# Performance work log

Hardware: AMD Instinct MI355X
Metric: run time of the kernel (lower is better)

## Reference

```python
import jax, jax.numpy as jnp
import numpy as np

NU, NM, D, E = 100000, 20000, 128, 1000000


def _seg_mean(feats, idx, n):
    # scatter-mean: zero for nodes with no incoming edges (PyG semantics)
    s = jax.ops.segment_sum(feats, idx, num_segments=n)
    c = jax.ops.segment_sum(jnp.ones((idx.shape[0], 1), feats.dtype), idx, num_segments=n)
    return s / jnp.maximum(c, 1.0)


def _hetero_sage(xu, xm, e_src, e_dst, Wl_um, Wr_um, b_um, Wl_mu, Wr_mu, b_mu):
    # ('user','rates','movie'): aggregate user features at movies
    agg_m = _seg_mean(xu[e_src], e_dst, xm.shape[0])          # [Nm, D]
    out_m = agg_m @ Wl_um + b_um + xm @ Wr_um                  # [Nm, H]
    # ('movie','rev_rates','user'): aggregate movie features at users
    agg_u = _seg_mean(xm[e_dst], e_src, xu.shape[0])          # [Nu, D]
    out_u = agg_u @ Wl_mu + b_mu + xu @ Wr_mu                  # [Nu, H]
    return out_u, out_m


def setup_inputs() -> dict:
    key = jax.random.key(0)
    ks = jax.random.split(key, 20)
    glorot = lambda k: (jax.random.normal(k, (D, D), jnp.float32) / np.sqrt(D)).astype(jnp.float32)
    inp = {
        "x_user": jax.random.normal(ks[0], (NU, D), jnp.float32),
        "x_movie": jax.random.normal(ks[1], (NM, D), jnp.float32),
        "edge_src": jax.random.randint(ks[2], (E,), 0, NU),
        "edge_dst": jax.random.randint(ks[3], (E,), 0, NM),
    }
    names = ["Wl1_um", "Wr1_um", "Wl1_mu", "Wr1_mu", "Wl2_um", "Wr2_um", "Wl2_mu", "Wr2_mu"]
    for i, n in enumerate(names):
        inp[n] = glorot(ks[4 + i])
    inp["b1_um"] = jnp.zeros((D,), jnp.float32)
    inp["b1_mu"] = jnp.zeros((D,), jnp.float32)
    inp["b2_um"] = jnp.zeros((D,), jnp.float32)
    inp["b2_mu"] = jnp.zeros((D,), jnp.float32)
    return inp


def reference(x_user, x_movie, Wl1_um, Wr1_um, Wl1_mu, Wr1_mu, Wl2_um, Wr2_um, Wl2_mu, Wr2_mu, b1_um, b1_mu, b2_um, b2_mu, edge_src, edge_dst):
    # layer 1 + relu (dropout = identity in eval) + residual
    h1_u, h1_m = _hetero_sage(x_user, x_movie, edge_src, edge_dst,
                              Wl1_um, Wr1_um, b1_um, Wl1_mu, Wr1_mu, b1_mu)
    r_u = x_user + jax.nn.relu(h1_u)
    r_m = x_movie + jax.nn.relu(h1_m)
    # layer 2 (dropout = identity in eval)
    out_u, out_m = _hetero_sage(r_u, r_m, edge_src, edge_dst,
                                Wl2_um, Wr2_um, b2_um, Wl2_mu, Wr2_mu, b2_mu)
    return out_u, out_m
```

## Files before the change

kernel.cpp:

```cpp
#include <hip/hip_runtime.h>
#include <stdint.h>

typedef unsigned short u16;
typedef unsigned int u32;
typedef __attribute__((ext_vector_type(8))) short short8;
typedef __attribute__((ext_vector_type(4))) float f32x4;

__device__ __forceinline__ u16 f2bf(float f) {
    u32 x = __float_as_uint(f);
    u32 r = x + 0x7FFFu + ((x >> 16) & 1u);
    return (u16)(r >> 16);
}
__device__ __forceinline__ u32 pack2bf(float a, float b) {
    return (u32)f2bf(a) | ((u32)f2bf(b) << 16);
}
__device__ __forceinline__ float bflo(u32 w) { return __uint_as_float(w << 16); }
__device__ __forceinline__ float bfhi(u32 w) { return __uint_as_float(w & 0xFFFF0000u); }

__global__ __launch_bounds__(256)
void hist_rank(const int* __restrict__ src, const int* __restrict__ dst,
               int* __restrict__ cnt, int* __restrict__ ranku,
               int* __restrict__ rankm, int E, int nu, int nm) {
    int e = blockIdx.x * 256 + threadIdx.x;
    if (e >= E) return;
    int s = src[e], d = dst[e];
    if ((unsigned)s < (unsigned)nu && (unsigned)d < (unsigned)nm) {
        ranku[e] = atomicAdd(&cnt[s], 1);
        rankm[e] = atomicAdd(&cnt[nu + d], 1);
    } else {
        ranku[e] = -1;
    }
}

__global__ __launch_bounds__(256)
void scan_partial(const int* __restrict__ cnt, int* __restrict__ bsum, int n) {
    __shared__ int s[256];
    const int tid = threadIdx.x;
    int base = blockIdx.x * 4096 + tid * 16;
    int sum = 0;
#pragma unroll
    for (int k = 0; k < 16; ++k) {
        int i = base + k;
        if (i < n) sum += cnt[i];
    }
    s[tid] = sum;
    __syncthreads();
    for (int d = 128; d > 0; d >>= 1) {
        if (tid < d) s[tid] += s[tid + d];
        __syncthreads();
    }
    if (tid == 0) bsum[blockIdx.x] = s[0];
}

__global__ __launch_bounds__(64)
void scan_top(int* __restrict__ bsum, int nb, int* __restrict__ off, int n) {
    if (threadIdx.x == 0) {
        int run = 0;
        for (int b = 0; b < nb; ++b) { int v = bsum[b]; bsum[b] = run; run += v; }
        off[n] = run;
    }
}

__global__ __launch_bounds__(256)
void scan_apply(const int* __restrict__ cnt, const int* __restrict__ bsum,
                int* __restrict__ off, int n) {
    __shared__ int s[256];
    const int tid = threadIdx.x;
    int base = blockIdx.x * 4096 + tid * 16;
    int v[16];
    int sum = 0;
#pragma unroll
    for (int k = 0; k < 16; ++k) {
        int i = base + k;
        v[k] = (i < n) ? cnt[i] : 0;
        sum += v[k];
    }
    s[tid] = sum;
    __syncthreads();
    for (int d = 1; d < 256; d <<= 1) {
        int t = (tid >= d) ? s[tid - d] : 0;
        __syncthreads();
        s[tid] += t;
        __syncthreads();
    }
    int run = bsum[blockIdx.x] + s[tid] - sum;
#pragma unroll
    for (int k = 0; k < 16; ++k) {
        int i = base + k;
        if (i < n) off[i] = run;
        run += v[k];
    }
}

__global__ __launch_bounds__(256)
void fill_pos(const int* __restrict__ src, const int* __restrict__ dst,
              const int* __restrict__ ranku, const int* __restrict__ rankm,
              const int* __restrict__ off, int* __restrict__ nbr,
              int E, int nu) {
    int e = blockIdx.x * 256 + threadIdx.x;
    if (e >= E) return;
    int ru = ranku[e];
    if (ru < 0) return;
    int s = src[e], d = dst[e];
    nbr[off[s] + ru] = d;
    nbr[off[nu + d] + rankm[e]] = s;
}

__global__ __launch_bounds__(256)
void to_bf16(const float* __restrict__ in, u32* __restrict__ out, int n64) {
    int i = blockIdx.x * 256 + threadIdx.x;
    if (i < n64) {
        float2 v = ((const float2*)in)[i];
        out[i] = pack2bf(v.x, v.y);
    }
}

__global__ __launch_bounds__(64)
void wprep(const float* __restrict__ Wl, const float* __restrict__ Wr,
           u16* __restrict__ out) {
    const int bid = blockIdx.x;
    const int t = bid >> 3, s = bid & 7;
    const int lane = threadIdx.x;
    const int n = t * 16 + (lane & 15);
    const int k0 = s * 32 + (lane >> 4) * 8;
    u16 v[8];
#pragma unroll
    for (int j = 0; j < 8; ++j) {
        int k = k0 + j;
        float f = (k < 128) ? Wl[k * 128 + n] : Wr[(k - 128) * 128 + n];
        v[j] = f2bf(f);
    }
    *(short8*)(out + ((size_t)(t * 8 + s) * 64 + lane) * 8) = *(short8*)v;
}

template <int L1>
__global__ __launch_bounds__(256)
void fused_update(const u32* __restrict__ featb, const float* __restrict__ xf,
                  const u32* __restrict__ xb,
                  const int* __restrict__ off, const int* __restrict__ nbr,
                  const u16* __restrict__ wt, const float* __restrict__ bias,
                  void* __restrict__ outp, int N) {
    __shared__ u32 sVb[16][132];
    __shared__ float sX[16][130];
    const int tid = threadIdx.x;
    const int lane = tid & 63;
    const int wave = tid >> 6;
    const int base = blockIdx.x * 16;

    for (int c = 0; c < 4; ++c) {
        const int i = wave * 4 + c;
        const int n = base + i;
        if (n < N) {
            const int b = off[n], e = off[n + 1];
            float a0x = 0.f, a0y = 0.f, a1x = 0.f, a1y = 0.f;
            float a2x = 0.f, a2y = 0.f, a3x = 0.f, a3y = 0.f;
            int t = b;
            for (; t + 3 < e; t += 4) {
                int g0 = nbr[t], g1 = nbr[t + 1], g2 = nbr[t + 2], g3 = nbr[t + 3];
                u32 w0 = featb[(size_t)g0 * 64 + lane];
                u32 w1 = featb[(size_t)g1 * 64 + lane];
                u32 w2 = featb[(size_t)g2 * 64 + lane];
                u32 w3 = featb[(size_t)g3 * 64 + lane];
                a0x += bflo(w0); a0y += bfhi(w0);
                a1x += bflo(w1); a1y += bfhi(w1);
                a2x += bflo(w2); a2y += bfhi(w2);
                a3x += bflo(w3); a3y += bfhi(w3);
            }
            for (; t < e; ++t) {
                u32 w = featb[(size_t)nbr[t] * 64 + lane];
                a0x += bflo(w); a0y += bfhi(w);
            }
            const int dg = e - b;
            const float inv = 1.0f / (float)(dg > 1 ? dg : 1);
            const float mx = (a0x + a1x + a2x + a3x) * inv;
            const float my = (a0y + a1y + a2y + a3y) * inv;
            sVb[i][lane] = pack2bf(mx, my);
            if (L1) {
                const float2 xv = ((const float2*)xf)[(size_t)n * 64 + lane];
                sVb[i][64 + lane] = pack2bf(xv.x, xv.y);
                sX[i][2 * lane] = xv.x;
                sX[i][2 * lane + 1] = xv.y;
            } else {
                sVb[i][64 + lane] = xb[(size_t)n * 64 + lane];
            }
        } else {
            sVb[i][lane] = 0u;
            sVb[i][64 + lane] = 0u;
            if (L1) { sX[i][2 * lane] = 0.f; sX[i][2 * lane + 1] = 0.f; }
        }
    }
    __syncthreads();

    const int ml = lane & 15;
    const int quad = lane >> 4;
    const int t0 = wave * 2, t1 = wave * 2 + 1;
    const u16* sVbu = (const u16*)sVb;
    const short8* wtp = (const short8*)wt;

    f32x4 acc0 = {0.f, 0.f, 0.f, 0.f};
    f32x4 acc1 = {0.f, 0.f, 0.f, 0.f};
#pragma unroll
    for (int s = 0; s < 8; ++s) {
        short8 a = *(const short8*)(sVbu + (size_t)ml * 264 + s * 32 + quad * 8);
        short8 b0 = wtp[(size_t)(t0 * 8 + s) * 64 + lane];
        short8 b1 = wtp[(size_t)(t1 * 8 + s) * 64 + lane];
        acc0 = __builtin_amdgcn_mfma_f32_16x16x32_bf16(a, b0, acc0, 0, 0, 0);
        acc1 = __builtin_amdgcn_mfma_f32_16x16x32_bf16(a, b1, acc1, 0, 0, 0);
    }

    const int n0 = t0 * 16 + ml, n1 = t1 * 16 + ml;
    const float bj0 = bias[n0], bj1 = bias[n1];
#pragma unroll
    for (int r = 0; r < 4; ++r) {
        const int m = quad * 4 + r;
        const int node = base + m;
        if (node < N) {
            float h0 = acc0[r] + bj0;
            float h1 = acc1[r] + bj1;
            if (L1) {
                u16* ob = (u16*)outp;
                ob[(size_t)node * 128 + n0] = f2bf(sX[m][n0] + fmaxf(h0, 0.f));
                ob[(size_t)node * 128 + n1] = f2bf(sX[m][n1] + fmaxf(h1, 0.f));
            } else {
                float* o = (float*)outp;
                o[(size_t)node * 128 + n0] = h0;
                o[(size_t)node * 128 + n1] = h1;
            }
        }
    }
}

extern "C" void kernel_launch(void* const* d_in, const int* in_sizes, int n_in,
                              void* d_out, int out_size, void* d_ws, size_t ws_size,
                              hipStream_t stream) {
    const int nu = in_sizes[0] / 128;
    const int nm = in_sizes[1] / 128;
    const int E = in_sizes[2];

    const float* xu = (const float*)d_in[0];
    const float* xm = (const float*)d_in[1];
    const int* esrc = (const int*)d_in[2];
    const int* edst = (const int*)d_in[3];
    const float* Wl1_um = (const float*)d_in[4];
    const float* Wr1_um = (const float*)d_in[5];
    const float* Wl1_mu = (const float*)d_in[6];
    const float* Wr1_mu = (const float*)d_in[7];
    const float* Wl2_um = (const float*)d_in[8];
    const float* Wr2_um = (const float*)d_in[9];
    const float* Wl2_mu = (const float*)d_in[10];
    const float* Wr2_mu = (const float*)d_in[11];
    const float* b1_um = (const float*)d_in[12];
    const float* b1_mu = (const float*)d_in[13];
    const float* b2_um = (const float*)d_in[14];
    const float* b2_mu = (const float*)d_in[15];

    float* out_u = (float*)d_out;
    float* out_m = out_u + (size_t)nu * 128;

    const int ntot = nu + nm;
    const int NB = (ntot + 4095) / 4096;
    int* cnt = (int*)d_ws;
    int* off = cnt + ntot;
    int* bsum = off + ntot + 1;
    int* ranku = bsum + ((NB + 15) & ~15);
    int* rankm = ranku + E;
    int* nbr = rankm + E;
    size_t int_bytes = (size_t)((nbr + 2 * (size_t)E) - (int*)d_ws) * 4;
    size_t wt_off = (int_bytes + 63) & ~(size_t)63;
    u16* wt1_um = (u16*)((char*)d_ws + wt_off);
    u16* wt1_mu = wt1_um + 32768;
    u16* wt2_um = wt1_mu + 32768;
    u16* wt2_mu = wt2_um + 32768;
    u32* Abf = (u32*)((char*)d_ws + wt_off + 4 * 65536);
    u32* xmb = Abf + (size_t)nu * 64;
    u32* rmb = xmb + (size_t)nm * 64;

    const int eg = (E + 255) / 256;

    wprep<<<64, 64, 0, stream>>>(Wl1_um, Wr1_um, wt1_um);
    wprep<<<64, 64, 0, stream>>>(Wl1_mu, Wr1_mu, wt1_mu);
    wprep<<<64, 64, 0, stream>>>(Wl2_um, Wr2_um, wt2_um);
    wprep<<<64, 64, 0, stream>>>(Wl2_mu, Wr2_mu, wt2_mu);
    to_bf16<<<(nu * 64 + 255) / 256, 256, 0, stream>>>(xu, Abf, nu * 64);
    to_bf16<<<(nm * 64 + 255) / 256, 256, 0, stream>>>(xm, xmb, nm * 64);

    hipMemsetAsync(cnt, 0, (size_t)ntot * 4, stream);
    hist_rank<<<eg, 256, 0, stream>>>(esrc, edst, cnt, ranku, rankm, E, nu, nm);
    scan_partial<<<NB, 256, 0, stream>>>(cnt, bsum, ntot);
    scan_top<<<1, 64, 0, stream>>>(bsum, NB, off, ntot);
    scan_apply<<<NB, 256, 0, stream>>>(cnt, bsum, off, ntot);
    fill_pos<<<eg, 256, 0, stream>>>(esrc, edst, ranku, rankm, off, nbr, E, nu);

    const int gm = (nm + 15) / 16;
    const int gu = (nu + 15) / 16;

    fused_update<1><<<gm, 256, 0, stream>>>(
        Abf, xm, nullptr, off + nu, nbr, wt1_um, b1_um, rmb, nm);
    fused_update<1><<<gu, 256, 0, stream>>>(
        xmb, xu, nullptr, off, nbr, wt1_mu, b1_mu, Abf, nu);

    fused_update<0><<<gm, 256, 0, stream>>>(
        Abf, nullptr, rmb, off + nu, nbr, wt2_um, b2_um, out_m, nm);
    fused_update<0><<<gu, 256, 0, stream>>>(
        rmb, nullptr, Abf, off, nbr, wt2_mu, b2_mu, out_u, nu);
}
```

Before: 570.7 us.

## Merge prep kernels, drop scan_top, vectorize gather, 32-node tiles, dual layer-2 launch

Folds histogram, bf16 conversion and weight packing into one prep launch. The scan's top level is now computed redundantly inside scan_apply, which assumes at most 64 partial blocks. The neighbor gather now uses 16-byte loads with four edges per wave in parallel plus a shuffle reduction, and each block handles 32 nodes with four MFMA accumulators. The two layer-2 updates share one launch. The main target is launch overhead and gather memory efficiency, at the cost of more registers and an fp32 re-read of x in the layer-1 epilogue.

```diff
diff --git a/kernel.cpp b/kernel.cpp
--- a/kernel.cpp
+++ b/kernel.cpp
@@ -5,6 +5,7 @@
 typedef unsigned int u32;
 typedef __attribute__((ext_vector_type(8))) short short8;
 typedef __attribute__((ext_vector_type(4))) float f32x4;
+typedef __attribute__((ext_vector_type(4))) u32 u32x4;
 
 __device__ __forceinline__ u16 f2bf(float f) {
     u32 x = __float_as_uint(f);
@@ -17,18 +18,67 @@
 __device__ __forceinline__ float bflo(u32 w) { return __uint_as_float(w << 16); }
 __device__ __forceinline__ float bfhi(u32 w) { return __uint_as_float(w & 0xFFFF0000u); }
 
-__global__ __launch_bounds__(256)
-void hist_rank(const int* __restrict__ src, const int* __restrict__ dst,
-               int* __restrict__ cnt, int* __restrict__ ranku,
-               int* __restrict__ rankm, int E, int nu, int nm) {
-    int e = blockIdx.x * 256 + threadIdx.x;
-    if (e >= E) return;
-    int s = src[e], d = dst[e];
-    if ((unsigned)s < (unsigned)nu && (unsigned)d < (unsigned)nm) {
-        ranku[e] = atomicAdd(&cnt[s], 1);
-        rankm[e] = atomicAdd(&cnt[nu + d], 1);
+struct WPtrs {
+    const float* wl[4];
+    const float* wr[4];
+    u16* wout[4];
+};
+
+__global__ __launch_bounds__(256)
+void prep_kernel(const int* __restrict__ src, const int* __restrict__ dst,
+                 int* __restrict__ cnt, int* __restrict__ ranku,
+                 int* __restrict__ rankm, int E, int nu, int nm,
+                 const float* __restrict__ xu, const float* __restrict__ xm,
+                 u32* __restrict__ xub, u32* __restrict__ xmb,
+                 int eg, int cg, WPtrs wp) {
+    const int bid = blockIdx.x;
+    const int tid = threadIdx.x;
+    if (bid < eg) {
+        int e = bid * 256 + tid;
+        if (e < E) {
+            int s = src[e], d = dst[e];
+            if ((unsigned)s < (unsigned)nu && (unsigned)d < (unsigned)nm) {
+                ranku[e] = atomicAdd(&cnt[s], 1);
+                rankm[e] = atomicAdd(&cnt[nu + d], 1);
+            } else {
+                ranku[e] = -1;
+            }
+        }
+    } else if (bid < eg + cg) {
+        const int id = (bid - eg) * 1024 + tid * 4;
+        const int nuc = nu * 64;
+        const int tot = nuc + nm * 64;
+        if (id < tot) {
+            const float* fin;
+            u32* fout;
+            int rel;
+            if (id < nuc) { fin = xu; fout = xub; rel = id; }
+            else          { fin = xm; fout = xmb; rel = id - nuc; }
+            float4 p0 = ((const float4*)fin)[(rel >> 1)];
+            float4 p1 = ((const float4*)fin)[(rel >> 1) + 1];
+            u32x4 o = { pack2bf(p0.x, p0.y), pack2bf(p0.z, p0.w),
+                        pack2bf(p1.x, p1.y), pack2bf(p1.z, p1.w) };
+            *(u32x4*)(fout + rel) = o;
+        }
     } else {
-        ranku[e] = -1;
+        const int unit = (bid - eg - cg) * 4 + (tid >> 6);
+        if (unit < 256) {
+            const int stack = unit >> 6, r = unit & 63, t = r >> 3, s = r & 7;
+            const int lane = tid & 63;
+            const float* Wl = wp.wl[stack];
+            const float* Wr = wp.wr[stack];
+            u16* outw = wp.wout[stack];
+            const int n = t * 16 + (lane & 15);
+            const int k0 = s * 32 + (lane >> 4) * 8;
+            u16 v[8];
+#pragma unroll
+            for (int j = 0; j < 8; ++j) {
+                int k = k0 + j;
+                float f = (k < 128) ? Wl[k * 128 + n] : Wr[(k - 128) * 128 + n];
+                v[j] = f2bf(f);
+            }
+            *(short8*)(outw + ((size_t)(t * 8 + s) * 64 + lane) * 8) = *(short8*)v;
+        }
     }
 }
 
@@ -52,19 +102,12 @@
     if (tid == 0) bsum[blockIdx.x] = s[0];
 }
 
-__global__ __launch_bounds__(64)
-void scan_top(int* __restrict__ bsum, int nb, int* __restrict__ off, int n) {
-    if (threadIdx.x == 0) {
-        int run = 0;
-        for (int b = 0; b < nb; ++b) { int v = bsum[b]; bsum[b] = run; run += v; }
-        off[n] = run;
-    }
-}
-
 __global__ __launch_bounds__(256)
 void scan_apply(const int* __restrict__ cnt, const int* __restrict__ bsum,
-                int* __restrict__ off, int n) {
+                int* __restrict__ off, int n, int nb) {
     __shared__ int s[256];
+    __shared__ int sb[64];
+    __shared__ int pfx;
     const int tid = threadIdx.x;
     int base = blockIdx.x * 4096 + tid * 16;
     int v[16];
@@ -76,6 +119,7 @@
         sum += v[k];
     }
     s[tid] = sum;
+    if (tid < 64) sb[tid] = (tid < nb) ? bsum[tid] : 0;
     __syncthreads();
     for (int d = 1; d < 256; d <<= 1) {
         int t = (tid >= d) ? s[tid - d] : 0;
@@ -83,7 +127,14 @@
         s[tid] += t;
         __syncthreads();
     }
-    int run = bsum[blockIdx.x] + s[tid] - sum;
+    if (tid == 0) {
+        int p = 0;
+        for (int b2 = 0; b2 < (int)blockIdx.x; ++b2) p += sb[b2];
+        pfx = p;
+        if ((int)blockIdx.x == nb - 1) off[n] = p + s[255];
+    }
+    __syncthreads();
+    int run = pfx + s[tid] - sum;
 #pragma unroll
     for (int k = 0; k < 16; ++k) {
         int i = base + k;
@@ -106,128 +157,152 @@
     nbr[off[nu + d] + rankm[e]] = s;
 }
 
-__global__ __launch_bounds__(256)
-void to_bf16(const float* __restrict__ in, u32* __restrict__ out, int n64) {
-    int i = blockIdx.x * 256 + threadIdx.x;
-    if (i < n64) {
-        float2 v = ((const float2*)in)[i];
-        out[i] = pack2bf(v.x, v.y);
-    }
-}
-
-__global__ __launch_bounds__(64)
-void wprep(const float* __restrict__ Wl, const float* __restrict__ Wr,
-           u16* __restrict__ out) {
-    const int bid = blockIdx.x;
-    const int t = bid >> 3, s = bid & 7;
-    const int lane = threadIdx.x;
-    const int n = t * 16 + (lane & 15);
-    const int k0 = s * 32 + (lane >> 4) * 8;
-    u16 v[8];
-#pragma unroll
-    for (int j = 0; j < 8; ++j) {
-        int k = k0 + j;
-        float f = (k < 128) ? Wl[k * 128 + n] : Wr[(k - 128) * 128 + n];
-        v[j] = f2bf(f);
-    }
-    *(short8*)(out + ((size_t)(t * 8 + s) * 64 + lane) * 8) = *(short8*)v;
-}
-
 template <int L1>
-__global__ __launch_bounds__(256)
-void fused_update(const u32* __restrict__ featb, const float* __restrict__ xf,
-                  const u32* __restrict__ xb,
-                  const int* __restrict__ off, const int* __restrict__ nbr,
-                  const u16* __restrict__ wt, const float* __restrict__ bias,
-                  void* __restrict__ outp, int N) {
-    __shared__ u32 sVb[16][132];
-    __shared__ float sX[16][130];
+__device__ __forceinline__ void fused_body(
+    const u32* __restrict__ featb, const float* __restrict__ xf,
+    const u32* __restrict__ xb, const int* __restrict__ off,
+    const int* __restrict__ nbr, const u16* __restrict__ wt,
+    const float* __restrict__ bias, void* __restrict__ outp, int N, int blk) {
+    __shared__ u32 sVb[32][132];
     const int tid = threadIdx.x;
     const int lane = tid & 63;
     const int wave = tid >> 6;
-    const int base = blockIdx.x * 16;
-
-    for (int c = 0; c < 4; ++c) {
-        const int i = wave * 4 + c;
+    const int base = blk * 32;
+    const int q = lane >> 4;
+    const int cl = lane & 15;
+
+    for (int c = 0; c < 8; ++c) {
+        const int i = wave * 8 + c;
         const int n = base + i;
         if (n < N) {
             const int b = off[n], e = off[n + 1];
-            float a0x = 0.f, a0y = 0.f, a1x = 0.f, a1y = 0.f;
-            float a2x = 0.f, a2y = 0.f, a3x = 0.f, a3y = 0.f;
+            float a0 = 0.f, a1 = 0.f, a2 = 0.f, a3 = 0.f;
+            float a4 = 0.f, a5 = 0.f, a6 = 0.f, a7 = 0.f;
             int t = b;
-            for (; t + 3 < e; t += 4) {
-                int g0 = nbr[t], g1 = nbr[t + 1], g2 = nbr[t + 2], g3 = nbr[t + 3];
-                u32 w0 = featb[(size_t)g0 * 64 + lane];
-                u32 w1 = featb[(size_t)g1 * 64 + lane];
-                u32 w2 = featb[(size_t)g2 * 64 + lane];
-                u32 w3 = featb[(size_t)g3 * 64 + lane];
-                a0x += bflo(w0); a0y += bfhi(w0);
-                a1x += bflo(w1); a1y += bfhi(w1);
-                a2x += bflo(w2); a2y += bfhi(w2);
-                a3x += bflo(w3); a3y += bfhi(w3);
-            }
-            for (; t < e; ++t) {
-                u32 w = featb[(size_t)nbr[t] * 64 + lane];
-                a0x += bflo(w); a0y += bfhi(w);
-            }
+            for (; t + 15 < e; t += 16) {
+                int g0 = nbr[t + q];
+                int g1 = nbr[t + 4 + q];
+                int g2 = nbr[t + 8 + q];
+                int g3 = nbr[t + 12 + q];
+                u32x4 v0 = *(const u32x4*)(featb + (size_t)g0 * 64 + cl * 4);
+                u32x4 v1 = *(const u32x4*)(featb + (size_t)g1 * 64 + cl * 4);
+                u32x4 v2 = *(const u32x4*)(featb + (size_t)g2 * 64 + cl * 4);
+                u32x4 v3 = *(const u32x4*)(featb + (size_t)g3 * 64 + cl * 4);
+                a0 += bflo(v0.x); a1 += bfhi(v0.x); a2 += bflo(v0.y); a3 += bfhi(v0.y);
+                a4 += bflo(v0.z); a5 += bfhi(v0.z); a6 += bflo(v0.w); a7 += bfhi(v0.w);
+                a0 += bflo(v1.x); a1 += bfhi(v1.x); a2 += bflo(v1.y); a3 += bfhi(v1.y);
+                a4 += bflo(v1.z); a5 += bfhi(v1.z); a6 += bflo(v1.w); a7 += bfhi(v1.w);
+                a0 += bflo(v2.x); a1 += bfhi(v2.x); a2 += bflo(v2.y); a3 += bfhi(v2.y);
+                a4 += bflo(v2.z); a5 += bfhi(v2.z); a6 += bflo(v2.w); a7 += bfhi(v2.w);
+                a0 += bflo(v3.x); a1 += bfhi(v3.x); a2 += bflo(v3.y); a3 += bfhi(v3.y);
+                a4 += bflo(v3.z); a5 += bfhi(v3.z); a6 += bflo(v3.w); a7 += bfhi(v3.w);
+            }
+            for (; t < e; t += 4) {
+                int it = t + q;
+                if (it < e) {
+                    u32x4 v = *(const u32x4*)(featb + (size_t)nbr[it] * 64 + cl * 4);
+                    a0 += bflo(v.x); a1 += bfhi(v.x); a2 += bflo(v.y); a3 += bfhi(v.y);
+                    a4 += bflo(v.z); a5 += bfhi(v.z); a6 += bflo(v.w); a7 += bfhi(v.w);
+                }
+            }
+            a0 += __shfl_xor(a0, 16); a0 += __shfl_xor(a0, 32);
+            a1 += __shfl_xor(a1, 16); a1 += __shfl_xor(a1, 32);
+            a2 += __shfl_xor(a2, 16); a2 += __shfl_xor(a2, 32);
+            a3 += __shfl_xor(a3, 16); a3 += __shfl_xor(a3, 32);
+            a4 += __shfl_xor(a4, 16); a4 += __shfl_xor(a4, 32);
+            a5 += __shfl_xor(a5, 16); a5 += __shfl_xor(a5, 32);
+            a6 += __shfl_xor(a6, 16); a6 += __shfl_xor(a6, 32);
+            a7 += __shfl_xor(a7, 16); a7 += __shfl_xor(a7, 32);
             const int dg = e - b;
             const float inv = 1.0f / (float)(dg > 1 ? dg : 1);
-            const float mx = (a0x + a1x + a2x + a3x) * inv;
-            const float my = (a0y + a1y + a2y + a3y) * inv;
-            sVb[i][lane] = pack2bf(mx, my);
+            if (q == 0) {
+                u32x4 o = { pack2bf(a0 * inv, a1 * inv), pack2bf(a2 * inv, a3 * inv),
+                            pack2bf(a4 * inv, a5 * inv), pack2bf(a6 * inv, a7 * inv) };
+                *(u32x4*)&sVb[i][cl * 4] = o;
+            }
             if (L1) {
                 const float2 xv = ((const float2*)xf)[(size_t)n * 64 + lane];
                 sVb[i][64 + lane] = pack2bf(xv.x, xv.y);
-                sX[i][2 * lane] = xv.x;
-                sX[i][2 * lane + 1] = xv.y;
             } else {
                 sVb[i][64 + lane] = xb[(size_t)n * 64 + lane];
             }
         } else {
             sVb[i][lane] = 0u;
             sVb[i][64 + lane] = 0u;
-            if (L1) { sX[i][2 * lane] = 0.f; sX[i][2 * lane + 1] = 0.f; }
         }
     }
     __syncthreads();
 
-    const int ml = lane & 15;
-    const int quad = lane >> 4;
-    const int t0 = wave * 2, t1 = wave * 2 + 1;
+    const int t0 = wave * 2, t1 = t0 + 1;
     const u16* sVbu = (const u16*)sVb;
     const short8* wtp = (const short8*)wt;
 
-    f32x4 acc0 = {0.f, 0.f, 0.f, 0.f};
-    f32x4 acc1 = {0.f, 0.f, 0.f, 0.f};
+    f32x4 acc00 = {0.f, 0.f, 0.f, 0.f};
+    f32x4 acc01 = {0.f, 0.f, 0.f, 0.f};
+    f32x4 acc10 = {0.f, 0.f, 0.f, 0.f};
+    f32x4 acc11 = {0.f, 0.f, 0.f, 0.f};
 #pragma unroll
     for (int s = 0; s < 8; ++s) {
-        short8 a = *(const short8*)(sVbu + (size_t)ml * 264 + s * 32 + quad * 8);
+        short8 a0 = *(const short8*)(sVbu + (size_t)cl * 264 + s * 32 + q * 8);
+        short8 a1 = *(const short8*)(sVbu + (size_t)(16 + cl) * 264 + s * 32 + q * 8);
         short8 b0 = wtp[(size_t)(t0 * 8 + s) * 64 + lane];
         short8 b1 = wtp[(size_t)(t1 * 8 + s) * 64 + lane];
-        acc0 = __builtin_amdgcn_mfma_f32_16x16x32_bf16(a, b0, acc0, 0, 0, 0);
-        acc1 = __builtin_amdgcn_mfma_f32_16x16x32_bf16(a, b1, acc1, 0, 0, 0);
-    }
-
-    const int n0 = t0 * 16 + ml, n1 = t1 * 16 + ml;
+        acc00 = __builtin_amdgcn_mfma_f32_16x16x32_bf16(a0, b0, acc00, 0, 0, 0);
+        acc01 = __builtin_amdgcn_mfma_f32_16x16x32_bf16(a0, b1, acc01, 0, 0, 0);
+        acc10 = __builtin_amdgcn_mfma_f32_16x16x32_bf16(a1, b0, acc10, 0, 0, 0);
+        acc11 = __builtin_amdgcn_mfma_f32_16x16x32_bf16(a1, b1, acc11, 0, 0, 0);
+    }
+
+    const int n0 = t0 * 16 + cl, n1 = t1 * 16 + cl;
     const float bj0 = bias[n0], bj1 = bias[n1];
 #pragma unroll
-    for (int r = 0; r < 4; ++r) {
-        const int m = quad * 4 + r;
-        const int node = base + m;
-        if (node < N) {
-            float h0 = acc0[r] + bj0;
-            float h1 = acc1[r] + bj1;
-            if (L1) {
-                u16* ob = (u16*)outp;
-                ob[(size_t)node * 128 + n0] = f2bf(sX[m][n0] + fmaxf(h0, 0.f));
-                ob[(size_t)node * 128 + n1] = f2bf(sX[m][n1] + fmaxf(h1, 0.f));
-            } else {
-                float* o = (float*)outp;
-                o[(size_t)node * 128 + n0] = h0;
-                o[(size_t)node * 128 + n1] = h1;
-            }
-        }
-    }
+    for (int mt = 0; mt < 2; ++mt) {
+        const f32x4& c0 = mt ? acc10 : acc00;
+        const f32x4& c1 = mt ? acc11 : acc01;
+#pragma unroll
+        for (int r = 0; r < 4; ++r) {
+            const int m = mt * 16 + q * 4 + r;
+            const int node = base + m;
+            if (node < N) {
+                float h0 = c0[r] + bj0;
+                float h1 = c1[r] + bj1;
+                if (L1) {
+                    u16* ob = (u16*)outp;
+                    float x0 = xf[(size_t)node * 128 + n0];
+                    float x1 = xf[(size_t)node * 128 + n1];
+                    ob[(size_t)node * 128 + n0] = f2bf(x0 + fmaxf(h0, 0.f));
+                    ob[(size_t)node * 128 + n1] = f2bf(x1 + fmaxf(h1, 0.f));
+                } else {
+                    float* o = (float*)outp;
+                    o[(size_t)node * 128 + n0] = h0;
+                    o[(size_t)node * 128 + n1] = h1;
+                }
+            }
+        }
+    }
+}
+
+__global__ __launch_bounds__(256)
+void fused_l1(const u32* __restrict__ featb, const float* __restrict__ xf,
+              const int* __restrict__ off, const int* __restrict__ nbr,
+              const u16* __restrict__ wt, const float* __restrict__ bias,
+              void* __restrict__ outp, int N) {
+    fused_body<1>(featb, xf, nullptr, off, nbr, wt, bias, outp, N, blockIdx.x);
+}
+
+__global__ __launch_bounds__(256)
+void fused_l2_dual(const u32* __restrict__ Abf, const u32* __restrict__ rmb,
+                   const int* __restrict__ off, const int* __restrict__ nbr,
+                   const u16* __restrict__ wtm, const u16* __restrict__ wtu,
+                   const float* __restrict__ bm, const float* __restrict__ bu,
+                   float* __restrict__ outm, float* __restrict__ outu,
+                   int nm, int nu, int gm) {
+    if ((int)blockIdx.x < gm)
+        fused_body<0>(Abf, nullptr, rmb, off + nu, nbr, wtm, bm, outm, nm,
+                      blockIdx.x);
+    else
+        fused_body<0>(rmb, nullptr, Abf, off, nbr, wtu, bu, outu, nu,
+                      blockIdx.x - gm);
 }
 
 extern "C" void kernel_launch(void* const* d_in, const int* in_sizes, int n_in,
@@ -276,31 +351,30 @@
     u32* rmb = xmb + (size_t)nm * 64;
 
     const int eg = (E + 255) / 256;
-
-    wprep<<<64, 64, 0, stream>>>(Wl1_um, Wr1_um, wt1_um);
-    wprep<<<64, 64, 0, stream>>>(Wl1_mu, Wr1_mu, wt1_mu);
-    wprep<<<64, 64, 0, stream>>>(Wl2_um, Wr2_um, wt2_um);
-    wprep<<<64, 64, 0, stream>>>(Wl2_mu, Wr2_mu, wt2_mu);
-    to_bf16<<<(nu * 64 + 255) / 256, 256, 0, stream>>>(xu, Abf, nu * 64);
-    to_bf16<<<(nm * 64 + 255) / 256, 256, 0, stream>>>(xm, xmb, nm * 64);
+    const int cg = ((nu + nm) * 64 + 1023) / 1024;
+
+    WPtrs wp;
+    wp.wl[0] = Wl1_um; wp.wr[0] = Wr1_um; wp.wout[0] = wt1_um;
+    wp.wl[1] = Wl1_mu; wp.wr[1] = Wr1_mu; wp.wout[1] = wt1_mu;
+    wp.wl[2] = Wl2_um; wp.wr[2] = Wr2_um; wp.wout[2] = wt2_um;
+    wp.wl[3] = Wl2_mu; wp.wr[3] = Wr2_mu; wp.wout[3] = wt2_mu;
 
     hipMemsetAsync(cnt, 0, (size_t)ntot * 4, stream);
-    hist_rank<<<eg, 256, 0, stream>>>(esrc, edst, cnt, ranku, rankm, E, nu, nm);
+    prep_kernel<<<eg + cg + 64, 256, 0, stream>>>(
+        esrc, edst, cnt, ranku, rankm, E, nu, nm, xu, xm, Abf, xmb, eg, cg, wp);
     scan_partial<<<NB, 256, 0, stream>>>(cnt, bsum, ntot);
-    scan_top<<<1, 64, 0, stream>>>(bsum, NB, off, ntot);
-    scan_apply<<<NB, 256, 0, stream>>>(cnt, bsum, off, ntot);
+    scan_apply<<<NB, 256, 0, stream>>>(cnt, bsum, off, ntot, NB);
     fill_pos<<<eg, 256, 0, stream>>>(esrc, edst, ranku, rankm, off, nbr, E, nu);
 
-    const int gm = (nm + 15) / 16;
-    const int gu = (nu + 15) / 16;
-
-    fused_update<1><<<gm, 256, 0, stream>>>(
-        Abf, xm, nullptr, off + nu, nbr, wt1_um, b1_um, rmb, nm);
-    fused_update<1><<<gu, 256, 0, stream>>>(
-        xmb, xu, nullptr, off, nbr, wt1_mu, b1_mu, Abf, nu);
-
-    fused_update<0><<<gm, 256, 0, stream>>>(
-        Abf, nullptr, rmb, off + nu, nbr, wt2_um, b2_um, out_m, nm);
-    fused_update<0><<<gu, 256, 0, stream>>>(
-        rmb, nullptr, Abf, off, nbr, wt2_mu, b2_mu, out_u, nu);
-}
+    const int gm = (nm + 31) / 32;
+    const int gu = (nu + 31) / 32;
+
+    fused_l1<<<gm, 256, 0, stream>>>(Abf, xm, off + nu, nbr, wt1_um, b1_um,
+                                     rmb, nm);
+    fused_l1<<<gu, 256, 0, stream>>>(xmb, xu, off, nbr, wt1_mu, b1_mu,
+                                     Abf, nu);
+
+    fused_l2_dual<<<gm + gu, 256, 0, stream>>>(
+        Abf, rmb, off, nbr, wt2_um, wt2_mu, b2_um, b2_mu, out_m, out_u,
+        nm, nu, gm);
+}
```

After: 514.9 us. 1.11x faster.
